# Performance work log

Measured on AMD Instinct MI355X. Metric: run time of the kernel, lower is better.

## Reference

```python
import jax, jax.numpy as jnp
import numpy as np

EPS = 1e-6
GAIN = 0.3

def setup_inputs() -> dict:
    key = jax.random.key(0)
    k1, k2 = jax.random.split(key)
    B, C, H, W = 8, 1024, 64, 64
    C_MID = 8
    z = jax.random.normal(k1, (B, C, H, W), dtype=jnp.float32)
    # down conv weight (c_mid, c_in); up weight is its transpose (PCA-ish projector)
    W_down = jax.random.normal(k2, (C_MID, C), dtype=jnp.float32) / np.sqrt(C)
    return {"z": z, "W_down": W_down}

def reference(z, W_down):
    # GroupNorm(1, C, affine=False): normalize over (C,H,W) per sample
    mu = jnp.mean(z, axis=(1, 2, 3), keepdims=True)
    var = jnp.var(z, axis=(1, 2, 3), keepdims=True)
    x = (z - mu) * jax.lax.rsqrt(var + EPS)
    # 1x1 conv down: (B,C,H,W) x (M,C) -> (B,M,H,W)
    y = jnp.einsum('bchw,mc->bmhw', x, W_down)
    # 1x1 conv up with weight = down^T: (B,M,H,W) x (M,C) -> (B,C,H,W)
    r = jnp.einsum('bmhw,mc->bchw', y, W_down)
    return z + GAIN * r
```

## Files before the change

kernel.cpp:

```cpp
#include <hip/hip_runtime.h>
#include <math.h>

#define B   8
#define C   1024
#define M   8
#define HW  4096
#define EPS 1e-6f
#define GAIN 0.3f

#define NT  8
#define NC  8
#define HWT (HW/NT)
#define CCH (C/NC)
#define TPB 256

#define OFF_YZP   0
#define OFF_STATP (OFF_YZP + B*NC*M*HW)
#define OFF_STATS (OFF_STATP + B*NT*NC*2)
#define OFF_S     (OFF_STATS + B*2)
#define OFF_Y     (OFF_S + M)
#define WS_FLOATS (OFF_Y + B*M*HW)

__global__ __launch_bounds__(TPB) void k1_partial(const float* __restrict__ z,
                                                  const float* __restrict__ Wd,
                                                  float* __restrict__ ws) {
    int bid = blockIdx.x;
    int nc  = bid % NC;
    int t   = (bid / NC) % NT;
    int b   = bid / (NC * NT);
    int tid = threadIdx.x;
    int hw  = t * HWT + tid * 2;
    int c0  = nc * CCH;

    float2 ym[M];
#pragma unroll
    for (int m = 0; m < M; ++m) ym[m] = make_float2(0.f, 0.f);
    float su = 0.f, sq = 0.f;

    const float* zp = z + ((size_t)(b * C + c0)) * HW + hw;
#pragma unroll 4
    for (int ci = 0; ci < CCH; ++ci) {
        float2 v = *reinterpret_cast<const float2*>(zp + (size_t)ci * HW);
        su += v.x + v.y;
        sq += v.x * v.x + v.y * v.y;
        int c = c0 + ci;
#pragma unroll
        for (int m = 0; m < M; ++m) {
            float w = Wd[m * C + c];
            ym[m].x += w * v.x;
            ym[m].y += w * v.y;
        }
    }

    float* yzp = ws + OFF_YZP + ((size_t)(b * NC + nc) * M) * HW + hw;
#pragma unroll
    for (int m = 0; m < M; ++m)
        *reinterpret_cast<float2*>(yzp + (size_t)m * HW) = ym[m];

    __shared__ float red[2 * TPB];
    red[tid] = su;
    red[TPB + tid] = sq;
    __syncthreads();
    for (int s = TPB / 2; s > 0; s >>= 1) {
        if (tid < s) {
            red[tid] += red[tid + s];
            red[TPB + tid] += red[TPB + tid + s];
        }
        __syncthreads();
    }
    if (tid == 0) {
        float* st = ws + OFF_STATP + ((size_t)b * (NT * NC) + t * NC + nc) * 2;
        st[0] = red[0];
        st[1] = red[TPB];
    }
}

__global__ __launch_bounds__(512) void k2_finalize(const float* __restrict__ Wd,
                                                   float* __restrict__ ws) {
    int tid = threadIdx.x;
    int w   = tid >> 6;
    int l   = tid & 63;

    {
        const float* sp = ws + OFF_STATP + ((size_t)w * (NT * NC) + l) * 2;
        float su = sp[0], sq = sp[1];
#pragma unroll
        for (int o = 32; o > 0; o >>= 1) {
            su += __shfl_down(su, o);
            sq += __shfl_down(sq, o);
        }
        if (l == 0) {
            const float invN = 1.0f / (float)(C * HW);
            float mu  = su * invN;
            float var = sq * invN - mu * mu;
            float istd = 1.0f / sqrtf(var + EPS);
            ws[OFF_STATS + w * 2]     = mu;
            ws[OFF_STATS + w * 2 + 1] = istd;
        }
    }
    {
        float sm = 0.f;
#pragma unroll
        for (int k = 0; k < C / 64; ++k) sm += Wd[w * C + k * 64 + l];
#pragma unroll
        for (int o = 32; o > 0; o >>= 1) sm += __shfl_down(sm, o);
        if (l == 0) ws[OFF_S + w] = sm;
    }
}

__global__ __launch_bounds__(TPB) void k3_reduce_y(float* __restrict__ ws) {
    int gid = blockIdx.x * TPB + threadIdx.x;
    int hw2 = gid % (HW / 2);
    int rem = gid / (HW / 2);
    int m   = rem % M;
    int b   = rem / M;
    int hw  = hw2 * 2;

    float2 acc = make_float2(0.f, 0.f);
    const float* p = ws + OFF_YZP + ((size_t)b * NC * M + m) * HW + hw;
#pragma unroll
    for (int nc = 0; nc < NC; ++nc) {
        float2 v = *reinterpret_cast<const float2*>(p + (size_t)nc * M * HW);
        acc.x += v.x;
        acc.y += v.y;
    }
    float mu   = ws[OFF_STATS + b * 2];
    float istd = ws[OFF_STATS + b * 2 + 1];
    float sm   = ws[OFF_S + m];
    float2 y;
    y.x = istd * (acc.x - mu * sm);
    y.y = istd * (acc.y - mu * sm);
    *reinterpret_cast<float2*>(ws + OFF_Y + ((size_t)b * M + m) * HW + hw) = y;
}

__global__ __launch_bounds__(TPB) void k4_apply(const float* __restrict__ z,
                                                const float* __restrict__ Wd,
                                                const float* __restrict__ ws,
                                                float* __restrict__ out) {
    int bid = blockIdx.x;
    int nc  = bid % NC;
    int t   = (bid / NC) % NT;
    int b   = bid / (NC * NT);
    int tid = threadIdx.x;
    int hw  = t * HWT + tid * 2;
    int c0  = nc * CCH;

    float2 y[M];
    const float* yp = ws + OFF_Y + (size_t)b * M * HW + hw;
#pragma unroll
    for (int m = 0; m < M; ++m)
        y[m] = *reinterpret_cast<const float2*>(yp + (size_t)m * HW);

    const float* zp = z + ((size_t)(b * C + c0)) * HW + hw;
    float* op = out + ((size_t)(b * C + c0)) * HW + hw;
#pragma unroll 4
    for (int ci = 0; ci < CCH; ++ci) {
        float2 v = *reinterpret_cast<const float2*>(zp + (size_t)ci * HW);
        int c = c0 + ci;
        float rx = 0.f, ry = 0.f;
#pragma unroll
        for (int m = 0; m < M; ++m) {
            float w = Wd[m * C + c];
            rx += w * y[m].x;
            ry += w * y[m].y;
        }
        float2 o;
        o.x = v.x + GAIN * rx;
        o.y = v.y + GAIN * ry;
        *reinterpret_cast<float2*>(op + (size_t)ci * HW) = o;
    }
}

extern "C" void kernel_launch(void* const* d_in, const int* in_sizes, int n_in,
                              void* d_out, int out_size, void* d_ws, size_t ws_size,
                              hipStream_t stream) {
    const float* z  = (const float*)d_in[0];
    const float* Wd = (const float*)d_in[1];
    float* out = (float*)d_out;
    float* ws  = (float*)d_ws;

    dim3 blk(TPB);
    k1_partial<<<dim3(B * NT * NC), blk, 0, stream>>>(z, Wd, ws);
    k2_finalize<<<dim3(1), dim3(512), 0, stream>>>(Wd, ws);
    k3_reduce_y<<<dim3((B * M * HW / 2) / TPB), blk, 0, stream>>>(ws);
    k4_apply<<<dim3(B * NT * NC), blk, 0, stream>>>(z, Wd, ws, out);
}
```

Baseline: 73.96 us.

## Fuse finalize and y-reduction into apply kernel, widen to float4

Merges the stats-finalize and partial-y reduction kernels into the apply kernel, so two launches and the intermediate y round trip through workspace go away. Each apply block now recomputes the per-sample mean/istd, the per-m weight sums, and reduces the NC partial y slices itself. Both main kernels switch from float2 to float4 per thread, and the HW tiling drops from 8 to 4 tiles, which halves the block count to 256. The cost is redundant reduction work in every block and fewer blocks to spread across the CUs.

Result: slower. 92.11 us (+24.5%).

```diff
diff --git a/kernel.cpp b/kernel.cpp
--- a/kernel.cpp
+++ b/kernel.cpp
@@ -1,25 +1,22 @@
 #include <hip/hip_runtime.h>
 #include <math.h>
 
-#define B   8
-#define C   1024
-#define M   8
-#define HW  4096
-#define EPS 1e-6f
+#define B    8
+#define C    1024
+#define M    8
+#define HW   4096
+#define EPS  1e-6f
 #define GAIN 0.3f
 
-#define NT  8
-#define NC  8
-#define HWT (HW/NT)
-#define CCH (C/NC)
-#define TPB 256
+#define NT   4
+#define NC   8
+#define NP   (NT*NC)
+#define HWT  (HW/NT)
+#define CCH  (C/NC)
+#define TPB  256
 
 #define OFF_YZP   0
 #define OFF_STATP (OFF_YZP + B*NC*M*HW)
-#define OFF_STATS (OFF_STATP + B*NT*NC*2)
-#define OFF_S     (OFF_STATS + B*2)
-#define OFF_Y     (OFF_S + M)
-#define WS_FLOATS (OFF_Y + B*M*HW)
 
 __global__ __launch_bounds__(TPB) void k1_partial(const float* __restrict__ z,
                                                   const float* __restrict__ Wd,
@@ -29,33 +26,35 @@
     int t   = (bid / NC) % NT;
     int b   = bid / (NC * NT);
     int tid = threadIdx.x;
-    int hw  = t * HWT + tid * 2;
+    int hw  = t * HWT + tid * 4;
     int c0  = nc * CCH;
 
-    float2 ym[M];
+    float4 ym[M];
 #pragma unroll
-    for (int m = 0; m < M; ++m) ym[m] = make_float2(0.f, 0.f);
+    for (int m = 0; m < M; ++m) ym[m] = make_float4(0.f, 0.f, 0.f, 0.f);
     float su = 0.f, sq = 0.f;
 
     const float* zp = z + ((size_t)(b * C + c0)) * HW + hw;
-#pragma unroll 4
+#pragma unroll 2
     for (int ci = 0; ci < CCH; ++ci) {
-        float2 v = *reinterpret_cast<const float2*>(zp + (size_t)ci * HW);
-        su += v.x + v.y;
-        sq += v.x * v.x + v.y * v.y;
+        float4 v = *reinterpret_cast<const float4*>(zp + (size_t)ci * HW);
+        su += (v.x + v.y) + (v.z + v.w);
+        sq += v.x * v.x + v.y * v.y + v.z * v.z + v.w * v.w;
         int c = c0 + ci;
 #pragma unroll
         for (int m = 0; m < M; ++m) {
             float w = Wd[m * C + c];
             ym[m].x += w * v.x;
             ym[m].y += w * v.y;
+            ym[m].z += w * v.z;
+            ym[m].w += w * v.w;
         }
     }
 
     float* yzp = ws + OFF_YZP + ((size_t)(b * NC + nc) * M) * HW + hw;
 #pragma unroll
     for (int m = 0; m < M; ++m)
-        *reinterpret_cast<float2*>(yzp + (size_t)m * HW) = ym[m];
+        *reinterpret_cast<float4*>(yzp + (size_t)m * HW) = ym[m];
 
     __shared__ float red[2 * TPB];
     red[tid] = su;
@@ -69,21 +68,35 @@
         __syncthreads();
     }
     if (tid == 0) {
-        float* st = ws + OFF_STATP + ((size_t)b * (NT * NC) + t * NC + nc) * 2;
+        float* st = ws + OFF_STATP + ((size_t)b * NP + t * NC + nc) * 2;
         st[0] = red[0];
         st[1] = red[TPB];
     }
 }
 
-__global__ __launch_bounds__(512) void k2_finalize(const float* __restrict__ Wd,
-                                                   float* __restrict__ ws) {
+__global__ __launch_bounds__(TPB) void k2_apply(const float* __restrict__ z,
+                                                const float* __restrict__ Wd,
+                                                const float* __restrict__ ws,
+                                                float* __restrict__ out) {
+    int bid = blockIdx.x;
+    int nc  = bid % NC;
+    int t   = (bid / NC) % NT;
+    int b   = bid / (NC * NT);
     int tid = threadIdx.x;
-    int w   = tid >> 6;
+    int wv  = tid >> 6;
     int l   = tid & 63;
+    int hw  = t * HWT + tid * 4;
+    int c0  = nc * CCH;
 
-    {
-        const float* sp = ws + OFF_STATP + ((size_t)w * (NT * NC) + l) * 2;
-        float su = sp[0], sq = sp[1];
+    __shared__ float sh[2 + M];
+
+    if (wv == 0) {
+        float su = 0.f, sq = 0.f;
+        if (l < NP) {
+            const float* sp = ws + OFF_STATP + ((size_t)b * NP + l) * 2;
+            su = sp[0];
+            sq = sp[1];
+        }
 #pragma unroll
         for (int o = 32; o > 0; o >>= 1) {
             su += __shfl_down(su, o);
@@ -93,81 +106,73 @@
             const float invN = 1.0f / (float)(C * HW);
             float mu  = su * invN;
             float var = sq * invN - mu * mu;
-            float istd = 1.0f / sqrtf(var + EPS);
-            ws[OFF_STATS + w * 2]     = mu;
-            ws[OFF_STATS + w * 2 + 1] = istd;
+            sh[0] = mu;
+            sh[1] = 1.0f / sqrtf(var + EPS);
         }
     }
     {
-        float sm = 0.f;
+        float sm0 = 0.f, sm1 = 0.f;
 #pragma unroll
-        for (int k = 0; k < C / 64; ++k) sm += Wd[w * C + k * 64 + l];
+        for (int k = 0; k < C / 64; ++k) {
+            sm0 += Wd[wv * C + k * 64 + l];
+            sm1 += Wd[(wv + 4) * C + k * 64 + l];
+        }
 #pragma unroll
-        for (int o = 32; o > 0; o >>= 1) sm += __shfl_down(sm, o);
-        if (l == 0) ws[OFF_S + w] = sm;
+        for (int o = 32; o > 0; o >>= 1) {
+            sm0 += __shfl_down(sm0, o);
+            sm1 += __shfl_down(sm1, o);
+        }
+        if (l == 0) {
+            sh[2 + wv]     = sm0;
+            sh[2 + wv + 4] = sm1;
+        }
     }
-}
+    __syncthreads();
+    float mu   = sh[0];
+    float istd = sh[1];
 
-__global__ __launch_bounds__(TPB) void k3_reduce_y(float* __restrict__ ws) {
-    int gid = blockIdx.x * TPB + threadIdx.x;
-    int hw2 = gid % (HW / 2);
-    int rem = gid / (HW / 2);
-    int m   = rem % M;
-    int b   = rem / M;
-    int hw  = hw2 * 2;
-
-    float2 acc = make_float2(0.f, 0.f);
-    const float* p = ws + OFF_YZP + ((size_t)b * NC * M + m) * HW + hw;
+    float4 y[M];
 #pragma unroll
-    for (int nc = 0; nc < NC; ++nc) {
-        float2 v = *reinterpret_cast<const float2*>(p + (size_t)nc * M * HW);
-        acc.x += v.x;
-        acc.y += v.y;
+    for (int m = 0; m < M; ++m) y[m] = make_float4(0.f, 0.f, 0.f, 0.f);
+    const float* yzb = ws + OFF_YZP + (size_t)b * NC * M * HW + hw;
+#pragma unroll
+    for (int ncp = 0; ncp < NC; ++ncp) {
+#pragma unroll
+        for (int m = 0; m < M; ++m) {
+            float4 v = *reinterpret_cast<const float4*>(yzb + ((size_t)(ncp * M + m)) * HW);
+            y[m].x += v.x; y[m].y += v.y; y[m].z += v.z; y[m].w += v.w;
+        }
     }
-    float mu   = ws[OFF_STATS + b * 2];
-    float istd = ws[OFF_STATS + b * 2 + 1];
-    float sm   = ws[OFF_S + m];
-    float2 y;
-    y.x = istd * (acc.x - mu * sm);
-    y.y = istd * (acc.y - mu * sm);
-    *reinterpret_cast<float2*>(ws + OFF_Y + ((size_t)b * M + m) * HW + hw) = y;
-}
-
-__global__ __launch_bounds__(TPB) void k4_apply(const float* __restrict__ z,
-                                                const float* __restrict__ Wd,
-                                                const float* __restrict__ ws,
-                                                float* __restrict__ out) {
-    int bid = blockIdx.x;
-    int nc  = bid % NC;
-    int t   = (bid / NC) % NT;
-    int b   = bid / (NC * NT);
-    int tid = threadIdx.x;
-    int hw  = t * HWT + tid * 2;
-    int c0  = nc * CCH;
-
-    float2 y[M];
-    const float* yp = ws + OFF_Y + (size_t)b * M * HW + hw;
 #pragma unroll
-    for (int m = 0; m < M; ++m)
-        y[m] = *reinterpret_cast<const float2*>(yp + (size_t)m * HW);
+    for (int m = 0; m < M; ++m) {
+        float off = mu * sh[2 + m];
+        y[m].x = istd * (y[m].x - off);
+        y[m].y = istd * (y[m].y - off);
+        y[m].z = istd * (y[m].z - off);
+        y[m].w = istd * (y[m].w - off);
+    }
 
     const float* zp = z + ((size_t)(b * C + c0)) * HW + hw;
     float* op = out + ((size_t)(b * C + c0)) * HW + hw;
-#pragma unroll 4
+#pragma unroll 2
     for (int ci = 0; ci < CCH; ++ci) {
-        float2 v = *reinterpret_cast<const float2*>(zp + (size_t)ci * HW);
+        float4 v = *reinterpret_cast<const float4*>(zp + (size_t)ci * HW);
         int c = c0 + ci;
-        float rx = 0.f, ry = 0.f;
+        float rx = 0.f, ry = 0.f, rz = 0.f, rw = 0.f;
 #pragma unroll
         for (int m = 0; m < M; ++m) {
             float w = Wd[m * C + c];
             rx += w * y[m].x;
             ry += w * y[m].y;
+            rz += w * y[m].z;
+            rw += w * y[m].w;
         }
-        float2 o;
+        float4 o;
         o.x = v.x + GAIN * rx;
         o.y = v.y + GAIN * ry;
-        *reinterpret_cast<float2*>(op + (size_t)ci * HW) = o;
+        o.z = v.z + GAIN * rz;
+        o.w = v.w + GAIN * rw;
+        *reinterpret_cast<float4*>(op + (size_t)ci * HW) = o;
     }
 }
 
@@ -181,7 +186,5 @@
 
     dim3 blk(TPB);
     k1_partial<<<dim3(B * NT * NC), blk, 0, stream>>>(z, Wd, ws);
-    k2_finalize<<<dim3(1), dim3(512), 0, stream>>>(Wd, ws);
-    k3_reduce_y<<<dim3((B * M * HW / 2) / TPB), blk, 0, stream>>>(ws);
-    k4_apply<<<dim3(B * NT * NC), blk, 0, stream>>>(z, Wd, ws, out);
+    k2_apply<<<dim3(B * NT * NC), blk, 0, stream>>>(z, Wd, ws, out);
 }
```
